# Kernel optimization log

Hardware: AMD Instinct MI355X
Metric: run time of the kernel (lower is better)

## Reference

```python
import jax, jax.numpy as jnp
import numpy as np

B, N, D, H = 4, 2048, 256, 4
DH = D // H
LN_EPS = 1e-5


def setup_inputs() -> dict:
    key = jax.random.key(0)
    ks = jax.random.split(key, 8)
    x = jax.random.normal(ks[0], (B, N, D), dtype=jnp.float32)
    adj = jax.random.randint(ks[1], (N, N), 0, 2, dtype=jnp.int32)
    # parameters (PyTorch Linear stores W as [out, in]; we store [out,in] and apply x @ W.T)
    W = jax.random.normal(ks[2], (D, D), dtype=jnp.float32) * (1.0 / np.sqrt(D))
    a_src = jax.random.normal(ks[3], (H, DH), dtype=jnp.float32)
    a_dst = jax.random.normal(ks[4], (H, DH), dtype=jnp.float32)
    Wo = jax.random.normal(ks[5], (D, D), dtype=jnp.float32) * (1.0 / np.sqrt(D))
    bo = jnp.zeros((D,), dtype=jnp.float32)
    gamma = jnp.ones((D,), dtype=jnp.float32)
    beta = jnp.zeros((D,), dtype=jnp.float32)
    return {"x": x, "adj": adj, "W": W, "a_src": a_src, "a_dst": a_dst,
            "Wo": Wo, "bo": bo, "gamma": gamma, "beta": beta}


def _layer_norm(y, gamma, beta):
    mu = jnp.mean(y, axis=-1, keepdims=True)
    var = jnp.mean((y - mu) ** 2, axis=-1, keepdims=True)
    return (y - mu) * jax.lax.rsqrt(var + LN_EPS) * gamma + beta


def reference(x, adj, W, a_src, a_dst, Wo, bo, gamma, beta):
    # dropout in eval mode (identity)
    b, n, d = x.shape
    h = (x @ W.T).reshape(b, n, H, DH).transpose(0, 2, 1, 3)  # [B,H,N,DH]
    src = jnp.einsum('bhnd,hd->bhn', h, a_src)  # [B,H,N]
    dst = jnp.einsum('bhnd,hd->bhn', h, a_dst)  # [B,H,N]
    e = src[:, :, :, None] + dst[:, :, None, :]  # e[b,h,i,j] = src_i + dst_j
    e = jnp.where(e >= 0, e, 0.2 * e)  # leaky_relu(0.2)
    mask = (adj > 0)[None, None, :, :]
    e = jnp.where(mask, e, -jnp.inf)
    attn = jax.nn.softmax(e, axis=-1)  # [B,H,N,N]
    out = jnp.einsum('bhij,bhjd->bhid', attn, h)  # [B,H,N,DH]
    out = out.transpose(0, 2, 1, 3).reshape(b, n, d)
    out = out @ Wo.T + bo
    return _layer_norm(x + out, gamma, beta)
```

## Files before the change

kernel.cpp:

```cpp
#include <hip/hip_runtime.h>
#include <stdint.h>

#define NTOK 2048
#define DMODEL 256
#define NHEAD 4

typedef __attribute__((ext_vector_type(8))) short short8;
typedef __attribute__((ext_vector_type(4))) float f32x4;

#define MFMA16(a, b, c) __builtin_amdgcn_mfma_f32_16x16x32_bf16(a, b, c, 0, 0, 0)

#if __has_builtin(__builtin_amdgcn_exp2f)
#define EXP2(x) __builtin_amdgcn_exp2f(x)
#else
#define EXP2(x) __expf((x) * 0.6931471805599453f)
#endif

__device__ __forceinline__ unsigned short f2bf(float f) {
  union { float f; unsigned int u; } v; v.f = f;
  unsigned int r = v.u + 0x7FFFu + ((v.u >> 16) & 1u);
  return (unsigned short)(r >> 16);
}

__device__ __forceinline__ f32x4 zero4() {
  f32x4 v; v[0] = 0.f; v[1] = 0.f; v[2] = 0.f; v[3] = 0.f; return v;
}

__global__ void k_prep_pack(const float* __restrict__ x, const float* __restrict__ W,
                            const float* __restrict__ Wo, const int* __restrict__ adj,
                            unsigned short* __restrict__ xbf, unsigned short* __restrict__ Wbf,
                            unsigned short* __restrict__ Wobf,
                            unsigned long long* __restrict__ bits) {
  const int b = blockIdx.x;
  if (b < 2176) {
    int e = (b * 256 + threadIdx.x) * 4;
    const float* s; unsigned short* d; int off;
    if (e < 2097152)              { s = x;  d = xbf;  off = e; }
    else if (e < 2097152 + 65536) { s = W;  d = Wbf;  off = e - 2097152; }
    else                          { s = Wo; d = Wobf; off = e - 2162688; }
    float4 v = *(const float4*)(s + off);
    ushort4 o;
    o.x = f2bf(v.x); o.y = f2bf(v.y); o.z = f2bf(v.z); o.w = f2bf(v.w);
    *(ushort4*)(d + off) = o;
  } else {
    int g = (b - 2176) * 256 + threadIdx.x;
    int v = adj[g];
    unsigned long long m = __ballot(v > 0);
    if ((threadIdx.x & 63) == 0) bits[g >> 6] = m;
  }
}

__global__ void k_gemm1(const unsigned short* __restrict__ xbf, const unsigned short* __restrict__ Wbf,
                        const float* __restrict__ a_src, const float* __restrict__ a_dst,
                        unsigned short* __restrict__ hT, float* __restrict__ srcv,
                        float* __restrict__ dstv) {
  __shared__ float tile[64][65];
  __shared__ float reds[2][4][64];
  const int tid = threadIdx.x, lane = tid & 63, w = tid >> 6;
  const int g0 = blockIdx.x * 64;
  const int hh = blockIdx.y;
  const int n0 = hh * 64;
  const int l15 = lane & 15, kl = (lane >> 4) * 8;

  const unsigned short* arow = xbf + (size_t)(g0 + w * 16 + l15) * 256 + kl;
  const unsigned short* brow = Wbf + (size_t)(n0 + l15) * 256 + kl;

  f32x4 acc[4];
#pragma unroll
  for (int nf = 0; nf < 4; ++nf) acc[nf] = zero4();

#pragma unroll
  for (int k = 0; k < 256; k += 32) {
    short8 a = *(const short8*)(arow + k);
#pragma unroll
    for (int nf = 0; nf < 4; ++nf) {
      short8 b = *(const short8*)(brow + nf * 4096 + k);
      acc[nf] = MFMA16(a, b, acc[nf]);
    }
  }

  const int rbase = w * 16 + (lane >> 4) * 4;
#pragma unroll
  for (int nf = 0; nf < 4; ++nf)
#pragma unroll
    for (int r = 0; r < 4; ++r)
      tile[rbase + r][nf * 16 + l15] = acc[nf][r];
  __syncthreads();

  const int bh = (g0 >> 11) * NHEAD + hh;
  {
    const int dh = tid >> 2, nq = (tid & 3) * 16;
    unsigned short* dp = hT + ((size_t)bh * 64 + dh) * 2048 + (g0 & 2047) + nq;
    short8 v0, v1;
#pragma unroll
    for (int q = 0; q < 8; ++q) v0[q] = (short)f2bf(tile[nq + q][dh]);
#pragma unroll
    for (int q = 0; q < 8; ++q) v1[q] = (short)f2bf(tile[nq + 8 + q][dh]);
    *(short8*)dp = v0;
    *(short8*)(dp + 8) = v1;
  }
  {
    const int n_loc = tid & 63, q4 = tid >> 6;
    const float* as = a_src + hh * 64 + q4 * 16;
    const float* ad = a_dst + hh * 64 + q4 * 16;
    float ps = 0.f, pd = 0.f;
#pragma unroll
    for (int d2 = 0; d2 < 16; ++d2) {
      float hv = tile[n_loc][q4 * 16 + d2];
      ps += hv * as[d2];
      pd += hv * ad[d2];
    }
    reds[0][q4][n_loc] = ps;
    reds[1][q4][n_loc] = pd;
  }
  __syncthreads();
  if (tid < 64) {
    float s = reds[0][0][tid] + reds[0][1][tid] + reds[0][2][tid] + reds[0][3][tid];
    float d = reds[1][0][tid] + reds[1][1][tid] + reds[1][2][tid] + reds[1][3][tid];
    srcv[(size_t)bh * 2048 + (g0 & 2047) + tid] = s;
    dstv[(size_t)bh * 2048 + (g0 & 2047) + tid] = d;
  }
}

__global__ __launch_bounds__(512, 4) void k_attn(
    const unsigned short* __restrict__ hT, const float* __restrict__ srcv,
    const float* __restrict__ dstv, const unsigned long long* __restrict__ bits,
    unsigned short* __restrict__ attb) {
  __shared__ float dst_s[2048];
  __shared__ unsigned long long adjw[64][33];
  __shared__ float src_s[64];
  __shared__ float red[8];
  __shared__ unsigned short kv[2][8192];
  __shared__ float comb[2][64][40];

  const int tid = threadIdx.x, lane = tid & 63, w = tid >> 6;
  const int orig = blockIdx.x;
  const int lid = (orig & 7) * 64 + (orig >> 3);
  const int bh = lid >> 5;
  const int i0 = (lid & 31) * 64;
  const int rg = w & 1, js = w >> 1;
  const float LOG2E = 1.4426950408889634f;

  float lmax = -3.0e38f;
  {
    const float* dsrc = dstv + (size_t)bh * 2048;
    int idx = tid * 4;
    float4 v = *(const float4*)(dsrc + idx);
    v.x *= LOG2E; v.y *= LOG2E; v.z *= LOG2E; v.w *= LOG2E;
    *(float4*)(dst_s + idx) = v;
    lmax = fmaxf(fmaxf(v.x, v.y), fmaxf(v.z, v.w));
#pragma unroll
    for (int off = 32; off >= 1; off >>= 1) lmax = fmaxf(lmax, __shfl_xor(lmax, off));
    if (lane == 0) red[w] = lmax;
    if (tid < 64) src_s[tid] = srcv[(size_t)bh * 2048 + i0 + tid] * LOG2E;
#pragma unroll
    for (int t = 0; t < 4; ++t) {
      int q = tid + t * 512;
      adjw[q >> 5][q & 31] = bits[(size_t)(i0 + (q >> 5)) * 32 + (q & 31)];
    }
  }

  const unsigned short* hTb = hT + (size_t)bh * 131072;
  const int c0 = tid, c1 = tid + 512;
  const int dh0 = c0 >> 4, ci0 = c0 & 15;
  const int dh1 = c1 >> 4, ci1 = c1 & 15;
  const int wof0 = dh0 * 128 + ((ci0 ^ (dh0 & 7)) << 3);
  const int wof1 = dh1 * 128 + ((ci1 ^ (dh1 & 7)) << 3);
  short8 st0 = *(const short8*)(hTb + dh0 * 2048 + ci0 * 8);
  short8 st1 = *(const short8*)(hTb + dh1 * 2048 + ci1 * 8);
  *(short8*)(&kv[0][wof0]) = st0;
  *(short8*)(&kv[0][wof1]) = st1;
  __syncthreads();
  const float dmax = fmaxf(fmaxf(fmaxf(red[0], red[1]), fmaxf(red[2], red[3])),
                           fmaxf(fmaxf(red[4], red[5]), fmaxf(red[6], red[7])));

  const int l15 = lane & 15, klg = lane >> 4, kl = klg * 8;
  const float src0 = src_s[rg * 32 + l15];
  const float src1 = src_s[rg * 32 + 16 + l15];
  const float sa0 = src0 + dmax, sa1 = src1 + dmax;
  const float m0 = fmaxf(sa0, 0.2f * sa0);
  const float m1 = fmaxf(sa1, 0.2f * sa1);
  const int xm = l15 & 7;
  const int chunk = (((js * 4 + klg) ^ xm) << 3) + l15 * 128;
  const int il0 = rg * 32 + l15, il1 = il0 + 16;
  const int wsel = js >> 1, wsh = (js & 1) * 32 + kl;

  short8 ones;
#pragma unroll
  for (int q = 0; q < 8; ++q) ones[q] = (short)0x3F80;

  f32x4 acc[2][4], accs[2];
#pragma unroll
  for (int rh = 0; rh < 2; ++rh) {
    accs[rh] = zero4();
#pragma unroll
    for (int nf = 0; nf < 4; ++nf) acc[rh][nf] = zero4();
  }

  for (int t = 0; t < 16; ++t) {
    const int cur = t & 1;
    if (t < 15) {
      const unsigned short* src = hTb + (t + 1) * 128;
      st0 = *(const short8*)(src + dh0 * 2048 + ci0 * 8);
      st1 = *(const short8*)(src + dh1 * 2048 + ci1 * 8);
    }
    const unsigned short* kvb = kv[cur];
    short8 bf[4];
#pragma unroll
    for (int nf = 0; nf < 4; ++nf) bf[nf] = *(const short8*)(kvb + nf * 2048 + chunk);
    const float* dsb = dst_s + t * 128 + js * 32;
    float4 d0 = *(const float4*)(dsb + kl);
    float4 d1 = *(const float4*)(dsb + kl + 4);
    float dv[8] = {d0.x, d0.y, d0.z, d0.w, d1.x, d1.y, d1.z, d1.w};
#pragma unroll
    for (int rh = 0; rh < 2; ++rh) {
      const float src_i = rh ? src1 : src0;
      const float m = rh ? m1 : m0;
      const unsigned long long word = adjw[rh ? il1 : il0][2 * t + wsel];
      const unsigned int byte = (unsigned int)(word >> wsh) & 0xFFu;
      float p[8];
#pragma unroll
      for (int t8 = 0; t8 < 8; ++t8) {
        float e = src_i + dv[t8];
        e = fmaxf(e, 0.2f * e);
        float s = ((byte >> t8) & 1u) ? (e - m) : -3.0e38f;
        p[t8] = EXP2(s);
      }
      union { short8 s8; unsigned int u32[4]; } af;
#pragma unroll
      for (int q = 0; q < 4; ++q)
        asm("v_cvt_pk_bf16_f32 %0, %1, %2" : "=v"(af.u32[q]) : "v"(p[2 * q]), "v"(p[2 * q + 1]));
      accs[rh] = MFMA16(af.s8, ones, accs[rh]);
#pragma unroll
      for (int nf = 0; nf < 4; ++nf) acc[rh][nf] = MFMA16(af.s8, bf[nf], acc[rh][nf]);
    }
    if (t < 15) {
      unsigned short* kvn = kv[cur ^ 1];
      *(short8*)(&kvn[wof0]) = st0;
      *(short8*)(&kvn[wof1]) = st1;
    }
    __syncthreads();
  }

#pragma unroll 1
  for (int s = 1; s < 4; ++s) {
    if (js == s) {
#pragma unroll
      for (int rh = 0; rh < 2; ++rh) {
#pragma unroll
        for (int nf = 0; nf < 4; ++nf)
#pragma unroll
          for (int r = 0; r < 4; ++r) comb[rg][lane][rh * 20 + nf * 4 + r] = acc[rh][nf][r];
#pragma unroll
        for (int r = 0; r < 4; ++r) comb[rg][lane][rh * 20 + 16 + r] = accs[rh][r];
      }
    }
    __syncthreads();
    if (js == 0) {
#pragma unroll
      for (int rh = 0; rh < 2; ++rh) {
#pragma unroll
        for (int nf = 0; nf < 4; ++nf)
#pragma unroll
          for (int r = 0; r < 4; ++r) acc[rh][nf][r] += comb[rg][lane][rh * 20 + nf * 4 + r];
#pragma unroll
        for (int r = 0; r < 4; ++r) accs[rh][r] += comb[rg][lane][rh * 20 + 16 + r];
      }
    }
    __syncthreads();
  }

  if (js == 0) {
    const int rb = klg * 4;
    const int b = bh >> 2, hh2 = bh & 3;
#pragma unroll
    for (int rh = 0; rh < 2; ++rh) {
      float linv[4];
#pragma unroll
      for (int r = 0; r < 4; ++r) linv[r] = 1.f / accs[rh][r];
#pragma unroll
      for (int nf = 0; nf < 4; ++nf)
#pragma unroll
        for (int r = 0; r < 4; ++r) {
          int i = i0 + rg * 32 + rh * 16 + rb + r;
          size_t o = ((size_t)(b * 2048 + i)) * 256 + hh2 * 64 + nf * 16 + l15;
          attb[o] = f2bf(acc[rh][nf][r] * linv[r]);
        }
    }
  }
}

__global__ void k_gemm2(const unsigned short* __restrict__ attb, const unsigned short* __restrict__ Wobf,
                        const float* __restrict__ bo, const float* __restrict__ x,
                        const float* __restrict__ gamma, const float* __restrict__ beta,
                        float* __restrict__ out) {
  __shared__ float tile[32][260];
  const int tid = threadIdx.x, lane = tid & 63, w = tid >> 6;
  const int g0 = blockIdx.x * 32;
  const int l15 = lane & 15, kl = (lane >> 4) * 8;
  const int rw = (w & 1) * 16;
  const int cb = (w >> 1) * 128;

  const unsigned short* arow = attb + (size_t)(g0 + rw + l15) * 256 + kl;
  const unsigned short* brow = Wobf + (size_t)(cb + l15) * 256 + kl;

  f32x4 acc[8];
#pragma unroll
  for (int nf = 0; nf < 8; ++nf) acc[nf] = zero4();

#pragma unroll
  for (int k = 0; k < 256; k += 32) {
    short8 a = *(const short8*)(arow + k);
#pragma unroll
    for (int nf = 0; nf < 8; ++nf) {
      short8 b = *(const short8*)(brow + (size_t)nf * 4096 + k);
      acc[nf] = MFMA16(a, b, acc[nf]);
    }
  }

  const int rb = rw + (lane >> 4) * 4;
#pragma unroll
  for (int nf = 0; nf < 8; ++nf)
#pragma unroll
    for (int r = 0; r < 4; ++r) {
      int c = cb + nf * 16 + l15;
      tile[rb + r][c] = acc[nf][r] + bo[c];
    }
  __syncthreads();

  const float4 gv = *(const float4*)(gamma + lane * 4);
  const float4 bv = *(const float4*)(beta + lane * 4);
  for (int r = 0; r < 8; ++r) {
    const int gl = w * 8 + r;
    const size_t g = g0 + gl;
    float4 xv = *(const float4*)(x + g * 256 + lane * 4);
    float4 tv = *(float4*)(&tile[gl][lane * 4]);
    float v0 = tv.x + xv.x, v1 = tv.y + xv.y, v2 = tv.z + xv.z, v3 = tv.w + xv.w;
    float sum = v0 + v1 + v2 + v3;
    float sq = v0 * v0 + v1 * v1 + v2 * v2 + v3 * v3;
#pragma unroll
    for (int off = 32; off >= 1; off >>= 1) {
      sum += __shfl_xor(sum, off);
      sq += __shfl_xor(sq, off);
    }
    const float mu = sum * (1.f / 256.f);
    const float var = sq * (1.f / 256.f) - mu * mu;
    const float rs = rsqrtf(var + 1e-5f);
    float4 o;
    o.x = (v0 - mu) * rs * gv.x + bv.x;
    o.y = (v1 - mu) * rs * gv.y + bv.y;
    o.z = (v2 - mu) * rs * gv.z + bv.z;
    o.w = (v3 - mu) * rs * gv.w + bv.w;
    *(float4*)(out + g * 256 + lane * 4) = o;
  }
}

extern "C" void kernel_launch(void* const* d_in, const int* in_sizes, int n_in,
                              void* d_out, int out_size, void* d_ws, size_t ws_size,
                              hipStream_t stream) {
  const float* x      = (const float*)d_in[0];
  const int*   adj    = (const int*)d_in[1];
  const float* W      = (const float*)d_in[2];
  const float* a_src  = (const float*)d_in[3];
  const float* a_dst  = (const float*)d_in[4];
  const float* Wo     = (const float*)d_in[5];
  const float* bo     = (const float*)d_in[6];
  const float* gamma  = (const float*)d_in[7];
  const float* beta   = (const float*)d_in[8];
  float* out = (float*)d_out;

  char* ws = (char*)d_ws;
  unsigned short* xbf       = (unsigned short*)(ws);
  unsigned short* hT        = (unsigned short*)(ws + (4u << 20));
  unsigned short* attb      = (unsigned short*)(ws + (8u << 20));
  unsigned long long* bits  = (unsigned long long*)(ws + (12u << 20));
  unsigned short* Wbf       = (unsigned short*)(ws + (12u << 20) + (512u << 10));
  unsigned short* Wobf      = (unsigned short*)(ws + (12u << 20) + (640u << 10));
  float* srcv               = (float*)(ws + (12u << 20) + (768u << 10));
  float* dstv               = (float*)(ws + (12u << 20) + (896u << 10));

  k_prep_pack<<<18560, 256, 0, stream>>>(x, W, Wo, adj, xbf, Wbf, Wobf, bits);
  k_gemm1<<<dim3(128, 4), 256, 0, stream>>>(xbf, Wbf, a_src, a_dst, hT, srcv, dstv);
  k_attn<<<512, 512, 0, stream>>>(hT, srcv, dstv, bits, attb);
  k_gemm2<<<256, 256, 0, stream>>>(attb, Wobf, bo, x, gamma, beta, out);
}
```

Measured before the change: 65.49 us.

## Fuse bf16 conversion into GEMM loads and merge adjacency packing into GEMM1

Removes the separate prep kernel that converted x, W and Wo to bf16. The GEMMs now read fp32 directly and convert in registers with v_cvt_pk_bf16_f32. The adjacency bitmask packing moves into extra blocks of the first GEMM kernel, with four ballots per thread, saving a launch and the bf16 staging writes and reads. In exchange the GEMMs read twice as many bytes per operand, and weights are reconverted redundantly by every block.

```diff
diff --git a/kernel.cpp b/kernel.cpp
--- a/kernel.cpp
+++ b/kernel.cpp
@@ -26,44 +26,44 @@
   f32x4 v; v[0] = 0.f; v[1] = 0.f; v[2] = 0.f; v[3] = 0.f; return v;
 }
 
-__global__ void k_prep_pack(const float* __restrict__ x, const float* __restrict__ W,
-                            const float* __restrict__ Wo, const int* __restrict__ adj,
-                            unsigned short* __restrict__ xbf, unsigned short* __restrict__ Wbf,
-                            unsigned short* __restrict__ Wobf,
-                            unsigned long long* __restrict__ bits) {
-  const int b = blockIdx.x;
-  if (b < 2176) {
-    int e = (b * 256 + threadIdx.x) * 4;
-    const float* s; unsigned short* d; int off;
-    if (e < 2097152)              { s = x;  d = xbf;  off = e; }
-    else if (e < 2097152 + 65536) { s = W;  d = Wbf;  off = e - 2097152; }
-    else                          { s = Wo; d = Wobf; off = e - 2162688; }
-    float4 v = *(const float4*)(s + off);
-    ushort4 o;
-    o.x = f2bf(v.x); o.y = f2bf(v.y); o.z = f2bf(v.z); o.w = f2bf(v.w);
-    *(ushort4*)(d + off) = o;
-  } else {
-    int g = (b - 2176) * 256 + threadIdx.x;
-    int v = adj[g];
-    unsigned long long m = __ballot(v > 0);
-    if ((threadIdx.x & 63) == 0) bits[g >> 6] = m;
-  }
-}
-
-__global__ void k_gemm1(const unsigned short* __restrict__ xbf, const unsigned short* __restrict__ Wbf,
-                        const float* __restrict__ a_src, const float* __restrict__ a_dst,
-                        unsigned short* __restrict__ hT, float* __restrict__ srcv,
-                        float* __restrict__ dstv) {
+__device__ __forceinline__ short8 cvt8(const float* p) {
+  float4 lo = *(const float4*)p;
+  float4 hi = *(const float4*)(p + 4);
+  union { short8 s8; unsigned int u[4]; } r;
+  asm("v_cvt_pk_bf16_f32 %0, %1, %2" : "=v"(r.u[0]) : "v"(lo.x), "v"(lo.y));
+  asm("v_cvt_pk_bf16_f32 %0, %1, %2" : "=v"(r.u[1]) : "v"(lo.z), "v"(lo.w));
+  asm("v_cvt_pk_bf16_f32 %0, %1, %2" : "=v"(r.u[2]) : "v"(hi.x), "v"(hi.y));
+  asm("v_cvt_pk_bf16_f32 %0, %1, %2" : "=v"(r.u[3]) : "v"(hi.z), "v"(hi.w));
+  return r.s8;
+}
+
+__global__ __launch_bounds__(256) void k_g1p(
+    const float* __restrict__ x, const float* __restrict__ W,
+    const float* __restrict__ a_src, const float* __restrict__ a_dst,
+    const int* __restrict__ adj,
+    unsigned short* __restrict__ hT, float* __restrict__ srcv, float* __restrict__ dstv,
+    unsigned long long* __restrict__ bits) {
   __shared__ float tile[64][65];
   __shared__ float reds[2][4][64];
+  const int b = blockIdx.x;
+  if (b >= 512) {
+    const int base = (b - 512) * 1024 + threadIdx.x;
+#pragma unroll
+    for (int r = 0; r < 4; ++r) {
+      int g = base + r * 256;
+      unsigned long long m = __ballot(adj[g] > 0);
+      if ((threadIdx.x & 63) == 0) bits[g >> 6] = m;
+    }
+    return;
+  }
   const int tid = threadIdx.x, lane = tid & 63, w = tid >> 6;
-  const int g0 = blockIdx.x * 64;
-  const int hh = blockIdx.y;
+  const int g0 = (b & 127) * 64;
+  const int hh = b >> 7;
   const int n0 = hh * 64;
   const int l15 = lane & 15, kl = (lane >> 4) * 8;
 
-  const unsigned short* arow = xbf + (size_t)(g0 + w * 16 + l15) * 256 + kl;
-  const unsigned short* brow = Wbf + (size_t)(n0 + l15) * 256 + kl;
+  const float* arow = x + (size_t)(g0 + w * 16 + l15) * 256 + kl;
+  const float* brow = W + (size_t)(n0 + l15) * 256 + kl;
 
   f32x4 acc[4];
 #pragma unroll
@@ -71,11 +71,11 @@
 
 #pragma unroll
   for (int k = 0; k < 256; k += 32) {
-    short8 a = *(const short8*)(arow + k);
+    short8 a = cvt8(arow + k);
 #pragma unroll
     for (int nf = 0; nf < 4; ++nf) {
-      short8 b = *(const short8*)(brow + nf * 4096 + k);
-      acc[nf] = MFMA16(a, b, acc[nf]);
+      short8 bb = cvt8(brow + nf * 4096 + k);
+      acc[nf] = MFMA16(a, bb, acc[nf]);
     }
   }
 
@@ -290,7 +290,7 @@
   }
 }
 
-__global__ void k_gemm2(const unsigned short* __restrict__ attb, const unsigned short* __restrict__ Wobf,
+__global__ void k_gemm2(const unsigned short* __restrict__ attb, const float* __restrict__ Wo,
                         const float* __restrict__ bo, const float* __restrict__ x,
                         const float* __restrict__ gamma, const float* __restrict__ beta,
                         float* __restrict__ out) {
@@ -302,7 +302,7 @@
   const int cb = (w >> 1) * 128;
 
   const unsigned short* arow = attb + (size_t)(g0 + rw + l15) * 256 + kl;
-  const unsigned short* brow = Wobf + (size_t)(cb + l15) * 256 + kl;
+  const float* brow = Wo + (size_t)(cb + l15) * 256 + kl;
 
   f32x4 acc[8];
 #pragma unroll
@@ -313,8 +313,8 @@
     short8 a = *(const short8*)(arow + k);
 #pragma unroll
     for (int nf = 0; nf < 8; ++nf) {
-      short8 b = *(const short8*)(brow + (size_t)nf * 4096 + k);
-      acc[nf] = MFMA16(a, b, acc[nf]);
+      short8 bb = cvt8(brow + (size_t)nf * 4096 + k);
+      acc[nf] = MFMA16(a, bb, acc[nf]);
     }
   }
 
@@ -370,17 +370,13 @@
   float* out = (float*)d_out;
 
   char* ws = (char*)d_ws;
-  unsigned short* xbf       = (unsigned short*)(ws);
-  unsigned short* hT        = (unsigned short*)(ws + (4u << 20));
-  unsigned short* attb      = (unsigned short*)(ws + (8u << 20));
+  unsigned short* hT        = (unsigned short*)(ws);
+  unsigned short* attb      = (unsigned short*)(ws + (4u << 20));
   unsigned long long* bits  = (unsigned long long*)(ws + (12u << 20));
-  unsigned short* Wbf       = (unsigned short*)(ws + (12u << 20) + (512u << 10));
-  unsigned short* Wobf      = (unsigned short*)(ws + (12u << 20) + (640u << 10));
   float* srcv               = (float*)(ws + (12u << 20) + (768u << 10));
   float* dstv               = (float*)(ws + (12u << 20) + (896u << 10));
 
-  k_prep_pack<<<18560, 256, 0, stream>>>(x, W, Wo, adj, xbf, Wbf, Wobf, bits);
-  k_gemm1<<<dim3(128, 4), 256, 0, stream>>>(xbf, Wbf, a_src, a_dst, hT, srcv, dstv);
+  k_g1p<<<4608, 256, 0, stream>>>(x, W, a_src, a_dst, adj, hT, srcv, dstv, bits);
   k_attn<<<512, 512, 0, stream>>>(hT, srcv, dstv, bits, attb);
-  k_gemm2<<<256, 256, 0, stream>>>(attb, Wobf, bo, x, gamma, beta, out);
-}
+  k_gemm2<<<256, 256, 0, stream>>>(attb, Wo, bo, x, gamma, beta, out);
+}
```

Result: slower. 79.68 us (+21.7%).

## Factor attention exponentials into precomputed per-row and per-column terms

Applied to the files above, without the earlier changes.

Rewrites exp2(leaky(src+dst)-m) as a product of a per-row factor and a per-column factor, choosing between the positive and negative branches by comparing exp2(dst) with a per-row threshold. The per-column exponentials are computed once into shared memory, which removes the transcendental from the inner attention loop and leaves a compare, select and multiply. The kv and comb shared buffers are unioned to offset the extra shared-memory array. This doubles the shared-memory reads of column data per iteration and may lose accuracy or overflow/underflow for extreme scores, since the threshold exponent is clamped.

```diff
diff --git a/kernel.cpp b/kernel.cpp
--- a/kernel.cpp
+++ b/kernel.cpp
@@ -122,16 +122,21 @@
   }
 }
 
+union KvComb {
+  unsigned short kv[2][8192];
+  float comb[2][64][40];
+};
+
 __global__ __launch_bounds__(512, 4) void k_attn(
     const unsigned short* __restrict__ hT, const float* __restrict__ srcv,
     const float* __restrict__ dstv, const unsigned long long* __restrict__ bits,
     unsigned short* __restrict__ attb) {
-  __shared__ float dst_s[2048];
+  __shared__ float bB_s[2048];
+  __shared__ float dD_s[2048];
   __shared__ unsigned long long adjw[64][33];
   __shared__ float src_s[64];
   __shared__ float red[8];
-  __shared__ unsigned short kv[2][8192];
-  __shared__ float comb[2][64][40];
+  __shared__ KvComb u;
 
   const int tid = threadIdx.x, lane = tid & 63, w = tid >> 6;
   const int orig = blockIdx.x;
@@ -147,8 +152,13 @@
     int idx = tid * 4;
     float4 v = *(const float4*)(dsrc + idx);
     v.x *= LOG2E; v.y *= LOG2E; v.z *= LOG2E; v.w *= LOG2E;
-    *(float4*)(dst_s + idx) = v;
     lmax = fmaxf(fmaxf(v.x, v.y), fmaxf(v.z, v.w));
+    float4 Bv, Dv;
+    Bv.x = EXP2(v.x); Bv.y = EXP2(v.y); Bv.z = EXP2(v.z); Bv.w = EXP2(v.w);
+    Dv.x = EXP2(0.2f * v.x); Dv.y = EXP2(0.2f * v.y);
+    Dv.z = EXP2(0.2f * v.z); Dv.w = EXP2(0.2f * v.w);
+    *(float4*)(bB_s + idx) = Bv;
+    *(float4*)(dD_s + idx) = Dv;
 #pragma unroll
     for (int off = 32; off >= 1; off >>= 1) lmax = fmaxf(lmax, __shfl_xor(lmax, off));
     if (lane == 0) red[w] = lmax;
@@ -168,8 +178,8 @@
   const int wof1 = dh1 * 128 + ((ci1 ^ (dh1 & 7)) << 3);
   short8 st0 = *(const short8*)(hTb + dh0 * 2048 + ci0 * 8);
   short8 st1 = *(const short8*)(hTb + dh1 * 2048 + ci1 * 8);
-  *(short8*)(&kv[0][wof0]) = st0;
-  *(short8*)(&kv[0][wof1]) = st1;
+  *(short8*)(&u.kv[0][wof0]) = st0;
+  *(short8*)(&u.kv[0][wof1]) = st1;
   __syncthreads();
   const float dmax = fmaxf(fmaxf(fmaxf(red[0], red[1]), fmaxf(red[2], red[3])),
                            fmaxf(fmaxf(red[4], red[5]), fmaxf(red[6], red[7])));
@@ -180,6 +190,10 @@
   const float sa0 = src0 + dmax, sa1 = src1 + dmax;
   const float m0 = fmaxf(sa0, 0.2f * sa0);
   const float m1 = fmaxf(sa1, 0.2f * sa1);
+  const float A0 = EXP2(src0 - m0), C0 = EXP2(fmaf(0.2f, src0, -m0));
+  const float A1 = EXP2(src1 - m1), C1 = EXP2(fmaf(0.2f, src1, -m1));
+  const float thB0 = EXP2(fminf(fmaxf(-src0, -125.f), 125.f));
+  const float thB1 = EXP2(fminf(fmaxf(-src1, -125.f), 125.f));
   const int xm = l15 & 7;
   const int chunk = (((js * 4 + klg) ^ xm) << 3) + l15 * 128;
   const int il0 = rg * 32 + l15, il1 = il0 + 16;
@@ -204,27 +218,32 @@
       st0 = *(const short8*)(src + dh0 * 2048 + ci0 * 8);
       st1 = *(const short8*)(src + dh1 * 2048 + ci1 * 8);
     }
-    const unsigned short* kvb = kv[cur];
+    const unsigned short* kvb = u.kv[cur];
     short8 bf[4];
 #pragma unroll
     for (int nf = 0; nf < 4; ++nf) bf[nf] = *(const short8*)(kvb + nf * 2048 + chunk);
-    const float* dsb = dst_s + t * 128 + js * 32;
-    float4 d0 = *(const float4*)(dsb + kl);
-    float4 d1 = *(const float4*)(dsb + kl + 4);
-    float dv[8] = {d0.x, d0.y, d0.z, d0.w, d1.x, d1.y, d1.z, d1.w};
+    const int jo = t * 128 + js * 32 + kl;
+    float4 b0 = *(const float4*)(bB_s + jo);
+    float4 b1 = *(const float4*)(bB_s + jo + 4);
+    float4 e0 = *(const float4*)(dD_s + jo);
+    float4 e1 = *(const float4*)(dD_s + jo + 4);
+    float bv[8] = {b0.x, b0.y, b0.z, b0.w, b1.x, b1.y, b1.z, b1.w};
+    float dq[8] = {e0.x, e0.y, e0.z, e0.w, e1.x, e1.y, e1.z, e1.w};
 #pragma unroll
     for (int rh = 0; rh < 2; ++rh) {
-      const float src_i = rh ? src1 : src0;
-      const float m = rh ? m1 : m0;
+      const float Ar = rh ? A1 : A0;
+      const float Cr = rh ? C1 : C0;
+      const float th = rh ? thB1 : thB0;
       const unsigned long long word = adjw[rh ? il1 : il0][2 * t + wsel];
       const unsigned int byte = (unsigned int)(word >> wsh) & 0xFFu;
       float p[8];
 #pragma unroll
       for (int t8 = 0; t8 < 8; ++t8) {
-        float e = src_i + dv[t8];
-        e = fmaxf(e, 0.2f * e);
-        float s = ((byte >> t8) & 1u) ? (e - m) : -3.0e38f;
-        p[t8] = EXP2(s);
+        const bool pos = bv[t8] >= th;
+        const float X = pos ? Ar : Cr;
+        const float Y = pos ? bv[t8] : dq[t8];
+        const float pv = X * Y;
+        p[t8] = ((byte >> t8) & 1u) ? pv : 0.f;
       }
       union { short8 s8; unsigned int u32[4]; } af;
 #pragma unroll
@@ -235,7 +254,7 @@
       for (int nf = 0; nf < 4; ++nf) acc[rh][nf] = MFMA16(af.s8, bf[nf], acc[rh][nf]);
     }
     if (t < 15) {
-      unsigned short* kvn = kv[cur ^ 1];
+      unsigned short* kvn = u.kv[cur ^ 1];
       *(short8*)(&kvn[wof0]) = st0;
       *(short8*)(&kvn[wof1]) = st1;
     }
@@ -250,9 +269,9 @@
 #pragma unroll
         for (int nf = 0; nf < 4; ++nf)
 #pragma unroll
-          for (int r = 0; r < 4; ++r) comb[rg][lane][rh * 20 + nf * 4 + r] = acc[rh][nf][r];
-#pragma unroll
-        for (int r = 0; r < 4; ++r) comb[rg][lane][rh * 20 + 16 + r] = accs[rh][r];
+          for (int r = 0; r < 4; ++r) u.comb[rg][lane][rh * 20 + nf * 4 + r] = acc[rh][nf][r];
+#pragma unroll
+        for (int r = 0; r < 4; ++r) u.comb[rg][lane][rh * 20 + 16 + r] = accs[rh][r];
       }
     }
     __syncthreads();
@@ -262,9 +281,9 @@
 #pragma unroll
         for (int nf = 0; nf < 4; ++nf)
 #pragma unroll
-          for (int r = 0; r < 4; ++r) acc[rh][nf][r] += comb[rg][lane][rh * 20 + nf * 4 + r];
-#pragma unroll
-        for (int r = 0; r < 4; ++r) accs[rh][r] += comb[rg][lane][rh * 20 + 16 + r];
+          for (int r = 0; r < 4; ++r) acc[rh][nf][r] += u.comb[rg][lane][rh * 20 + nf * 4 + r];
+#pragma unroll
+        for (int r = 0; r < 4; ++r) accs[rh][r] += u.comb[rg][lane][rh * 20 + 16 + r];
       }
     }
     __syncthreads();
```

Result: slower. 69.09 us (+5.5%).

## Factor GAT exponentials into precomputed per-node terms and load pre-swizzled fragments from global

Applied to the files above, without the earlier changes.

The attention kernel now uses exp(leaky(s+d)-m) = A*exp(d) or C*exp(0.2d), picked per element by a threshold comparison. Per-column exponentials are precomputed once into shared memory, which takes the exp2 out of the inner loop. gemm1 writes hT in an MFMA-fragment-ready layout, so k_attn reads B fragments straight from global into registers, double-buffered, and drops the LDS staging and the per-tile __syncthreads. The risks are different numerics (exp(d) can overflow or underflow, and the clamp on the threshold matters) and higher global/L2 traffic, since every wave loads its own fragments.

```diff
diff --git a/kernel.cpp b/kernel.cpp
--- a/kernel.cpp
+++ b/kernel.cpp
@@ -52,7 +52,7 @@
 
 __global__ void k_gemm1(const unsigned short* __restrict__ xbf, const unsigned short* __restrict__ Wbf,
                         const float* __restrict__ a_src, const float* __restrict__ a_dst,
-                        unsigned short* __restrict__ hT, float* __restrict__ srcv,
+                        unsigned short* __restrict__ hTg, float* __restrict__ srcv,
                         float* __restrict__ dstv) {
   __shared__ float tile[64][65];
   __shared__ float reds[2][4][64];
@@ -90,7 +90,9 @@
   const int bh = (g0 >> 11) * NHEAD + hh;
   {
     const int dh = tid >> 2, nq = (tid & 3) * 16;
-    unsigned short* dp = hT + ((size_t)bh * 64 + dh) * 2048 + (g0 & 2047) + nq;
+    const int c = ((g0 & 2047) + nq) >> 5;
+    const int k0 = (nq & 16) >> 3;
+    unsigned short* dp = hTg + (size_t)bh * 131072 + c * 2048 + dh * 32 + k0 * 8;
     short8 v0, v1;
 #pragma unroll
     for (int q = 0; q < 8; ++q) v0[q] = (short)f2bf(tile[nq + q][dh]);
@@ -123,14 +125,14 @@
 }
 
 __global__ __launch_bounds__(512, 4) void k_attn(
-    const unsigned short* __restrict__ hT, const float* __restrict__ srcv,
+    const unsigned short* __restrict__ hTg, const float* __restrict__ srcv,
     const float* __restrict__ dstv, const unsigned long long* __restrict__ bits,
     unsigned short* __restrict__ attb) {
-  __shared__ float dst_s[2048];
+  __shared__ float bB_s[2048];
+  __shared__ float dD_s[2048];
   __shared__ unsigned long long adjw[64][33];
   __shared__ float src_s[64];
   __shared__ float red[8];
-  __shared__ unsigned short kv[2][8192];
   __shared__ float comb[2][64][40];
 
   const int tid = threadIdx.x, lane = tid & 63, w = tid >> 6;
@@ -147,8 +149,13 @@
     int idx = tid * 4;
     float4 v = *(const float4*)(dsrc + idx);
     v.x *= LOG2E; v.y *= LOG2E; v.z *= LOG2E; v.w *= LOG2E;
-    *(float4*)(dst_s + idx) = v;
     lmax = fmaxf(fmaxf(v.x, v.y), fmaxf(v.z, v.w));
+    float4 Bv, Dv;
+    Bv.x = EXP2(v.x); Bv.y = EXP2(v.y); Bv.z = EXP2(v.z); Bv.w = EXP2(v.w);
+    Dv.x = EXP2(0.2f * v.x); Dv.y = EXP2(0.2f * v.y);
+    Dv.z = EXP2(0.2f * v.z); Dv.w = EXP2(0.2f * v.w);
+    *(float4*)(bB_s + idx) = Bv;
+    *(float4*)(dD_s + idx) = Dv;
 #pragma unroll
     for (int off = 32; off >= 1; off >>= 1) lmax = fmaxf(lmax, __shfl_xor(lmax, off));
     if (lane == 0) red[w] = lmax;
@@ -159,17 +166,6 @@
       adjw[q >> 5][q & 31] = bits[(size_t)(i0 + (q >> 5)) * 32 + (q & 31)];
     }
   }
-
-  const unsigned short* hTb = hT + (size_t)bh * 131072;
-  const int c0 = tid, c1 = tid + 512;
-  const int dh0 = c0 >> 4, ci0 = c0 & 15;
-  const int dh1 = c1 >> 4, ci1 = c1 & 15;
-  const int wof0 = dh0 * 128 + ((ci0 ^ (dh0 & 7)) << 3);
-  const int wof1 = dh1 * 128 + ((ci1 ^ (dh1 & 7)) << 3);
-  short8 st0 = *(const short8*)(hTb + dh0 * 2048 + ci0 * 8);
-  short8 st1 = *(const short8*)(hTb + dh1 * 2048 + ci1 * 8);
-  *(short8*)(&kv[0][wof0]) = st0;
-  *(short8*)(&kv[0][wof1]) = st1;
   __syncthreads();
   const float dmax = fmaxf(fmaxf(fmaxf(red[0], red[1]), fmaxf(red[2], red[3])),
                            fmaxf(fmaxf(red[4], red[5]), fmaxf(red[6], red[7])));
@@ -180,11 +176,16 @@
   const float sa0 = src0 + dmax, sa1 = src1 + dmax;
   const float m0 = fmaxf(sa0, 0.2f * sa0);
   const float m1 = fmaxf(sa1, 0.2f * sa1);
-  const int xm = l15 & 7;
-  const int chunk = (((js * 4 + klg) ^ xm) << 3) + l15 * 128;
+  const float A0 = EXP2(src0 - m0), C0 = EXP2(fmaf(0.2f, src0, -m0));
+  const float A1 = EXP2(src1 - m1), C1 = EXP2(fmaf(0.2f, src1, -m1));
+  const float thB0 = EXP2(fminf(fmaxf(-src0, -125.f), 125.f));
+  const float thB1 = EXP2(fminf(fmaxf(-src1, -125.f), 125.f));
   const int il0 = rg * 32 + l15, il1 = il0 + 16;
   const int wsel = js >> 1, wsh = (js & 1) * 32 + kl;
 
+  const unsigned short* hgb = hTg + (size_t)bh * 131072;
+  const int fragoff = l15 * 32 + klg * 8;
+
   short8 ones;
 #pragma unroll
   for (int q = 0; q < 8; ++q) ones[q] = (short)0x3F80;
@@ -197,50 +198,77 @@
     for (int nf = 0; nf < 4; ++nf) acc[rh][nf] = zero4();
   }
 
-  for (int t = 0; t < 16; ++t) {
-    const int cur = t & 1;
-    if (t < 15) {
-      const unsigned short* src = hTb + (t + 1) * 128;
-      st0 = *(const short8*)(src + dh0 * 2048 + ci0 * 8);
-      st1 = *(const short8*)(src + dh1 * 2048 + ci1 * 8);
-    }
-    const unsigned short* kvb = kv[cur];
-    short8 bf[4];
-#pragma unroll
-    for (int nf = 0; nf < 4; ++nf) bf[nf] = *(const short8*)(kvb + nf * 2048 + chunk);
-    const float* dsb = dst_s + t * 128 + js * 32;
-    float4 d0 = *(const float4*)(dsb + kl);
-    float4 d1 = *(const float4*)(dsb + kl + 4);
-    float dv[8] = {d0.x, d0.y, d0.z, d0.w, d1.x, d1.y, d1.z, d1.w};
-#pragma unroll
-    for (int rh = 0; rh < 2; ++rh) {
-      const float src_i = rh ? src1 : src0;
-      const float m = rh ? m1 : m0;
-      const unsigned long long word = adjw[rh ? il1 : il0][2 * t + wsel];
-      const unsigned int byte = (unsigned int)(word >> wsh) & 0xFFu;
-      float p[8];
-#pragma unroll
-      for (int t8 = 0; t8 < 8; ++t8) {
-        float e = src_i + dv[t8];
-        e = fmaxf(e, 0.2f * e);
-        float s = ((byte >> t8) & 1u) ? (e - m) : -3.0e38f;
-        p[t8] = EXP2(s);
-      }
-      union { short8 s8; unsigned int u32[4]; } af;
-#pragma unroll
-      for (int q = 0; q < 4; ++q)
-        asm("v_cvt_pk_bf16_f32 %0, %1, %2" : "=v"(af.u32[q]) : "v"(p[2 * q]), "v"(p[2 * q + 1]));
-      accs[rh] = MFMA16(af.s8, ones, accs[rh]);
-#pragma unroll
-      for (int nf = 0; nf < 4; ++nf) acc[rh][nf] = MFMA16(af.s8, bf[nf], acc[rh][nf]);
-    }
-    if (t < 15) {
-      unsigned short* kvn = kv[cur ^ 1];
-      *(short8*)(&kvn[wof0]) = st0;
-      *(short8*)(&kvn[wof1]) = st1;
-    }
-    __syncthreads();
-  }
+  short8 pA0, pA1, pA2, pA3, pB0, pB1, pB2, pB3;
+  {
+    const unsigned short* kp = hgb + js * 2048 + fragoff;
+    pA0 = *(const short8*)(kp);
+    pA1 = *(const short8*)(kp + 512);
+    pA2 = *(const short8*)(kp + 1024);
+    pA3 = *(const short8*)(kp + 1536);
+  }
+
+#define GAT_TILE(T, C0_, C1_, C2_, C3_, N0_, N1_, N2_, N3_)                       \
+  {                                                                               \
+    if ((T) < 15) {                                                               \
+      const unsigned short* kp = hgb + (((T) + 1) * 4 + js) * 2048 + fragoff;     \
+      N0_ = *(const short8*)(kp);                                                 \
+      N1_ = *(const short8*)(kp + 512);                                           \
+      N2_ = *(const short8*)(kp + 1024);                                          \
+      N3_ = *(const short8*)(kp + 1536);                                          \
+    }                                                                             \
+    const int jo = (T) * 128 + js * 32 + kl;                                      \
+    float4 b0 = *(const float4*)(bB_s + jo);                                      \
+    float4 b1 = *(const float4*)(bB_s + jo + 4);                                  \
+    float4 e0 = *(const float4*)(dD_s + jo);                                      \
+    float4 e1 = *(const float4*)(dD_s + jo + 4);                                  \
+    float bv[8] = {b0.x, b0.y, b0.z, b0.w, b1.x, b1.y, b1.z, b1.w};               \
+    float dq[8] = {e0.x, e0.y, e0.z, e0.w, e1.x, e1.y, e1.z, e1.w};               \
+    const unsigned long long w0_ = adjw[il0][2 * (T) + wsel];                     \
+    const unsigned long long w1_ = adjw[il1][2 * (T) + wsel];                     \
+    {                                                                             \
+      const unsigned int byte = (unsigned int)(w0_ >> wsh) & 0xFFu;               \
+      float p[8];                                                                 \
+      _Pragma("unroll") for (int t8 = 0; t8 < 8; ++t8) {                          \
+        const bool pos = bv[t8] >= thB0;                                          \
+        const float pv = (pos ? A0 : C0) * (pos ? bv[t8] : dq[t8]);               \
+        p[t8] = ((byte >> t8) & 1u) ? pv : 0.f;                                   \
+      }                                                                           \
+      union { short8 s8; unsigned int u32[4]; } af;                               \
+      _Pragma("unroll") for (int q = 0; q < 4; ++q)                               \
+        asm("v_cvt_pk_bf16_f32 %0, %1, %2"                                       \
+            : "=v"(af.u32[q]) : "v"(p[2 * q]), "v"(p[2 * q + 1]));                \
+      accs[0] = MFMA16(af.s8, ones, accs[0]);                                     \
+      acc[0][0] = MFMA16(af.s8, C0_, acc[0][0]);                                  \
+      acc[0][1] = MFMA16(af.s8, C1_, acc[0][1]);                                  \
+      acc[0][2] = MFMA16(af.s8, C2_, acc[0][2]);                                  \
+      acc[0][3] = MFMA16(af.s8, C3_, acc[0][3]);                                  \
+    }                                                                             \
+    {                                                                             \
+      const unsigned int byte = (unsigned int)(w1_ >> wsh) & 0xFFu;               \
+      float p[8];                                                                 \
+      _Pragma("unroll") for (int t8 = 0; t8 < 8; ++t8) {                          \
+        const bool pos = bv[t8] >= thB1;                                          \
+        const float pv = (pos ? A1 : C1) * (pos ? bv[t8] : dq[t8]);               \
+        p[t8] = ((byte >> t8) & 1u) ? pv : 0.f;                                   \
+      }                                                                           \
+      union { short8 s8; unsigned int u32[4]; } af;                               \
+      _Pragma("unroll") for (int q = 0; q < 4; ++q)                               \
+        asm("v_cvt_pk_bf16_f32 %0, %1, %2"                                       \
+            : "=v"(af.u32[q]) : "v"(p[2 * q]), "v"(p[2 * q + 1]));                \
+      accs[1] = MFMA16(af.s8, ones, accs[1]);                                     \
+      acc[1][0] = MFMA16(af.s8, C0_, acc[1][0]);                                  \
+      acc[1][1] = MFMA16(af.s8, C1_, acc[1][1]);                                  \
+      acc[1][2] = MFMA16(af.s8, C2_, acc[1][2]);                                  \
+      acc[1][3] = MFMA16(af.s8, C3_, acc[1][3]);                                  \
+    }                                                                             \
+  }
+
+#pragma unroll 1
+  for (int tt = 0; tt < 16; tt += 2) {
+    GAT_TILE(tt, pA0, pA1, pA2, pA3, pB0, pB1, pB2, pB3);
+    GAT_TILE(tt + 1, pB0, pB1, pB2, pB3, pA0, pA1, pA2, pA3);
+  }
+#undef GAT_TILE
 
 #pragma unroll 1
   for (int s = 1; s < 4; ++s) {
@@ -371,7 +399,7 @@
 
   char* ws = (char*)d_ws;
   unsigned short* xbf       = (unsigned short*)(ws);
-  unsigned short* hT        = (unsigned short*)(ws + (4u << 20));
+  unsigned short* hTg       = (unsigned short*)(ws + (4u << 20));
   unsigned short* attb      = (unsigned short*)(ws + (8u << 20));
   unsigned long long* bits  = (unsigned long long*)(ws + (12u << 20));
   unsigned short* Wbf       = (unsigned short*)(ws + (12u << 20) + (512u << 10));
@@ -380,7 +408,7 @@
   float* dstv               = (float*)(ws + (12u << 20) + (896u << 10));
 
   k_prep_pack<<<18560, 256, 0, stream>>>(x, W, Wo, adj, xbf, Wbf, Wobf, bits);
-  k_gemm1<<<dim3(128, 4), 256, 0, stream>>>(xbf, Wbf, a_src, a_dst, hT, srcv, dstv);
-  k_attn<<<512, 512, 0, stream>>>(hT, srcv, dstv, bits, attb);
+  k_gemm1<<<dim3(128, 4), 256, 0, stream>>>(xbf, Wbf, a_src, a_dst, hTg, srcv, dstv);
+  k_attn<<<512, 512, 0, stream>>>(hTg, srcv, dstv, bits, attb);
   k_gemm2<<<256, 256, 0, stream>>>(attb, Wobf, bo, x, gamma, beta, out);
 }
```

New measurement: 60.92 us. -7.0%, faster.
